# Performance work log

Measured on AMD Instinct MI355X. Metric: run time of the kernel, lower is better.

## Reference

```python
import jax, jax.numpy as jnp
import numpy as np

B, T = 4, 32768
NM = 80      # n_mels
RC = 120     # residual_channels
SC = 240     # skip_channels
NB = 16      # num_blocks
ND = 8       # num_dilations
NC = 256     # num_classes


def setup_inputs() -> dict:
    key = jax.random.key(0)
    ks = jax.random.split(key, 18)
    s = 0.05
    return {
        "wav": jax.random.normal(ks[0], (B, 1, T), dtype=jnp.float32),
        "cond": jax.random.normal(ks[1], (B, NM, T), dtype=jnp.float32),
        "wav_w": jax.random.normal(ks[2], (RC, 1)) * s,
        "wav_b": jnp.zeros((RC,), jnp.float32),
        "cond_w": jax.random.normal(ks[3], (NB, 2 * RC, NM)) * s,
        "cond_b": jnp.zeros((NB, 2 * RC), jnp.float32),
        "dil_w": jax.random.normal(ks[4], (NB, 2 * RC, RC, 2)) * s,
        "dil_b": jnp.zeros((NB, 2 * RC), jnp.float32),
        "skip_w": jax.random.normal(ks[5], (NB, SC, RC)) * s,
        "skip_b": jnp.zeros((NB, SC), jnp.float32),
        "res_w": jax.random.normal(ks[6], (NB, RC, RC)) * s,
        "res_b": jnp.zeros((NB, RC), jnp.float32),
        "out_w": jax.random.normal(ks[7], (NC, SC)) * s,
        "out_b": jnp.zeros((NC,), jnp.float32),
        "end_w": jax.random.normal(ks[8], (NC, NC)) * s,
        "end_b": jnp.zeros((NC,), jnp.float32),
    }


def _conv1x1(w, b, x):
    # w: [O, I], x: [B, I, T] -> [B, O, T]
    return jnp.einsum('oi,bit->bot', w, x) + b[:, None]


def reference(wav, cond, wav_w, wav_b, cond_w, cond_b, dil_w, dil_b,
              skip_w, skip_b, res_w, res_b, out_w, out_b, end_w, end_b):
    Tlen = wav.shape[-1]
    res = _conv1x1(wav_w, wav_b, wav)                      # [B, RC, T]
    skip_sum = jnp.zeros((wav.shape[0], SC, Tlen), wav.dtype)
    for i in range(NB):
        d = 2 ** (i % ND)
        # torch: Conv1d(k=2, dilation=d, padding=d) then [:, :, :-d] == causal conv
        # out[t] = W0 @ x[t-d] + W1 @ x[t]
        x_shift = jnp.pad(res, ((0, 0), (0, 0), (d, 0)))[:, :, :Tlen]
        g = (jnp.einsum('oi,bit->bot', dil_w[i, :, :, 0], x_shift)
             + jnp.einsum('oi,bit->bot', dil_w[i, :, :, 1], res)
             + dil_b[i][:, None]
             + _conv1x1(cond_w[i], cond_b[i], cond))        # [B, 2*RC, T]
        # first RC channels -> tanh branch, second RC -> sigmoid branch
        out = jnp.tanh(g[:, :RC]) * jax.nn.sigmoid(g[:, RC:])
        skip_sum = skip_sum + _conv1x1(skip_w[i], skip_b[i], out)
        res = _conv1x1(res_w[i], res_b[i], out) + res
    o = _conv1x1(out_w, out_b, jax.nn.relu(skip_sum))       # [B, NC, T]
    end = _conv1x1(end_w, end_b, jax.nn.relu(o))            # [B, NC, T]
    return end
```

## Files before the change

kernel.cpp:

```cpp
#include <hip/hip_runtime.h>
#include <hip/hip_fp16.h>


#define BSZ  4
#define TLEN 32768
#define NMEL 80
#define RCH  120
#define SCH  240
#define NBLK 16
#define NCLS 256
#define CP   128
#define CC   96
#define TSB  128
#define TSF  64
#define OUTS 136
#define XES  264

typedef __attribute__((ext_vector_type(8))) short short8;
typedef __attribute__((ext_vector_type(4))) float floatx4;
#define MFMA16 __builtin_amdgcn_mfma_f32_16x16x32_bf16

__device__ __forceinline__ float bf2f(unsigned short u) {
    return __uint_as_float(((unsigned)u) << 16);
}
__device__ __forceinline__ unsigned short f2bf(float f) {
    unsigned x = __float_as_uint(f);
    return (unsigned short)((x + 0x7fffu + ((x >> 16) & 1u)) >> 16);
}
__device__ __forceinline__ float h2f(unsigned short u) {
    return __half2float(__ushort_as_half(u));
}
__device__ __forceinline__ unsigned short f2h(float f) {
    return __half_as_ushort(__float2half(f));
}
__device__ __forceinline__ float tanh_ap(float x) {
    x = fminf(fmaxf(x, -18.f), 18.f);
    float e = __expf(2.f * x);
    return (e - 1.f) / (e + 1.f);
}
__device__ __forceinline__ float sigm_ap(float x) {
    x = fminf(fmaxf(x, -30.f), 30.f);
    return 1.f / (1.f + __expf(-x));
}

#define FR_BLK   257
#define FR_TOT   4368
#define NWELEM   (FR_TOT * 512)
#define BIA_BLK  608
#define NBELEM   (NBLK * BIA_BLK + 512)

__global__ void k_packw(const float* __restrict__ dil_w, const float* __restrict__ cond_w,
                        const float* __restrict__ skip_w, const float* __restrict__ res_w,
                        const float* __restrict__ out_w,  const float* __restrict__ end_w,
                        unsigned short* __restrict__ dst) {
    int idx = blockIdx.x * 256 + threadIdx.x;
    if (idx >= NWELEM) return;
    int fid = idx >> 9;
    int r   = idx & 511;
    int lane = r >> 3, j = r & 7;
    int m16 = lane & 15, q = lane >> 4;
    float v = 0.f;
    if (fid < NBLK * FR_BLK) {
        int blk = fid / FR_BLK, f = fid % FR_BLK;
        if (f < 165) {
            int mt = f / 11, ks = f % 11;
            int row = 16 * mt + m16;
            int kk  = ks * 32 + q * 8 + j;
            int c = row >> 1, br = row & 1;
            int srow = c + 120 * br;
            if (kk < 128) {
                if (kk < 120) v = dil_w[((size_t)(blk * 240 + srow) * 120 + kk) * 2 + 0];
            } else if (kk < 256) {
                int ch = kk - 128;
                if (ch < 120) v = dil_w[((size_t)(blk * 240 + srow) * 120 + ch) * 2 + 1];
            } else {
                int ch = kk - 256;
                if (ch < 80) v = cond_w[(size_t)(blk * 240 + srow) * 80 + ch];
            }
        } else if (f < 225) {
            int f2 = f - 165, mt = f2 / 4, ks = f2 % 4;
            int row = 16 * mt + m16;
            int kk = ks * 32 + q * 8 + j;
            if (kk < 120) v = skip_w[(size_t)(blk * 240 + row) * 120 + kk];
        } else {
            int f2 = f - 225, mt = f2 / 4, ks = f2 % 4;
            int row = 16 * mt + m16;
            int kk = ks * 32 + q * 8 + j;
            if (row < 120 && kk < 120) v = res_w[(size_t)(blk * 120 + row) * 120 + kk];
        }
    } else if (fid < NBLK * FR_BLK + 128) {
        int f = fid - NBLK * FR_BLK, mt = f / 8, ks = f % 8;
        int row = 16 * mt + m16;
        int kk = ks * 32 + q * 8 + j;
        if (kk < 240) v = out_w[(size_t)row * 240 + kk];
    } else {
        int f = fid - NBLK * FR_BLK - 128, mt = f / 8, ks = f % 8;
        int row = 16 * mt + m16;
        int kk = ks * 32 + q * 8 + j;
        v = end_w[(size_t)row * 256 + kk];
    }
    dst[idx] = f2bf(v);
}

__global__ void k_packb(const float* __restrict__ dil_b, const float* __restrict__ cond_b,
                        const float* __restrict__ skip_b, const float* __restrict__ res_b,
                        const float* __restrict__ out_b,  const float* __restrict__ end_b,
                        float* __restrict__ dst) {
    int idx = blockIdx.x * 256 + threadIdx.x;
    if (idx >= NBELEM) return;
    float v;
    if (idx < NBLK * BIA_BLK) {
        int blk = idx / BIA_BLK, f = idx % BIA_BLK;
        if (f < 240) {
            int c = f >> 1, br = f & 1;
            int srow = c + 120 * br;
            v = dil_b[blk * 240 + srow] + cond_b[blk * 240 + srow];
        } else if (f < 480) {
            v = skip_b[blk * 240 + (f - 240)];
        } else {
            int rr = f - 480;
            v = rr < 120 ? res_b[blk * 120 + rr] : 0.f;
        }
    } else {
        int f = idx - NBLK * BIA_BLK;
        v = f < 256 ? out_b[f] : end_b[f - 256];
    }
    dst[idx] = v;
}

__global__ void k_init2(const float* __restrict__ wav, const float* __restrict__ wav_w,
                        const float* __restrict__ wav_b, unsigned short* __restrict__ res) {
    int idx = blockIdx.x * 256 + threadIdx.x;
    float wv = wav[idx];
    unsigned* dst = (unsigned*)(res + (size_t)idx * CP);
#pragma unroll
    for (int c = 0; c < RCH; c += 2) {
        float v0 = wav_w[c] * wv + wav_b[c];
        float v1 = wav_w[c + 1] * wv + wav_b[c + 1];
        dst[c >> 1] = (unsigned)f2bf(v0) | ((unsigned)f2bf(v1) << 16);
    }
#pragma unroll
    for (int c = RCH; c < CP; c += 2) dst[c >> 1] = 0u;
}

__global__ __launch_bounds__(256) void k_packc(const float* __restrict__ cond,
                                               unsigned short* __restrict__ dst) {
    __shared__ unsigned short CT[64 * CC];
    const int tid = threadIdx.x;
    const int t0 = blockIdx.x * 64;
    const int b = blockIdx.y;
    for (int i = tid; i < NMEL * 64; i += 256) {
        int c = i >> 6, tt = i & 63;
        CT[tt * CC + c] = f2bf(cond[((size_t)b * NMEL + c) * TLEN + t0 + tt]);
    }
    for (int i = tid; i < (CC - NMEL) * 64; i += 256) {
        int c = NMEL + (i >> 6), tt = i & 63;
        CT[tt * CC + c] = 0;
    }
    __syncthreads();
    unsigned* dp = (unsigned*)(dst + ((size_t)b * TLEN + t0) * CC);
    const unsigned* sp = (const unsigned*)CT;
    for (int i = tid; i < 64 * (CC / 2); i += 256) dp[i] = sp[i];
}

template <bool HF>
__global__ __launch_bounds__(256, 2) void k_block4(
    const unsigned short* __restrict__ resIn,
    unsigned short* __restrict__ resOut,
    const unsigned short* __restrict__ condp,
    void* __restrict__ skipPtr,
    const unsigned short* __restrict__ wp,
    const float* __restrict__ bp,
    int d) {
    __shared__ __align__(16) unsigned short OUT[TSB * OUTS];
    __shared__ __align__(16) float BIAS[BIA_BLK];

    const int tid = threadIdx.x;
    const int lane = tid & 63;
    const int n = lane & 15, q = lane >> 4;
    const int w = __builtin_amdgcn_readfirstlane(tid >> 6);
    const int t0 = blockIdx.x * TSB;
    const int b = blockIdx.y;
    const size_t bT = (size_t)b * TLEN;

    for (int i = tid; i < BIA_BLK; i += 256) BIAS[i] = bp[i];
    for (int i = tid; i < TSB * 8; i += 256) {
        int col = i >> 3, ch = RCH + (i & 7);
        OUT[col * OUTS + ch] = 0;
    }

    const int mtb = w * 4;
    const int mtn = (w == 3) ? 3 : 4;
    const unsigned short* resb = resIn + bT * CP;
    const unsigned short* conb = condp + bT * CC;

    floatx4 acc[4][8];
#pragma unroll
    for (int mi = 0; mi < 4; mi++)
#pragma unroll
        for (int nt = 0; nt < 8; nt++) acc[mi][nt] = (floatx4){0.f, 0.f, 0.f, 0.f};

    for (int ks = 0; ks < 11; ks++) {
        short8 Bf[8];
        if (ks < 8) {
            const int dd = (ks < 4) ? d : 0;
            const int kl = (ks & 3) * 32 + q * 8;
            if (t0 >= TSB || dd == 0) {
#pragma unroll
                for (int nt = 0; nt < 8; nt++) {
                    int t = t0 + nt * 16 + n - dd;
                    Bf[nt] = *(const short8*)(resb + (size_t)t * CP + kl);
                }
            } else {
#pragma unroll
                for (int nt = 0; nt < 8; nt++) {
                    int t = t0 + nt * 16 + n - dd;
                    int tc = t < 0 ? 0 : t;
                    short8 v = *(const short8*)(resb + (size_t)tc * CP + kl);
                    if (t < 0) v = (short8){0, 0, 0, 0, 0, 0, 0, 0};
                    Bf[nt] = v;
                }
            }
        } else {
            const int kl = (ks - 8) * 32 + q * 8;
#pragma unroll
            for (int nt = 0; nt < 8; nt++) {
                int t = t0 + nt * 16 + n;
                Bf[nt] = *(const short8*)(conb + (size_t)t * CC + kl);
            }
        }
#pragma unroll
        for (int mi = 0; mi < 4; mi++) {
            if (mi < mtn) {
                short8 A = *(const short8*)(wp + ((size_t)((mtb + mi) * 11 + ks) * 64 + lane) * 8);
#pragma unroll
                for (int nt = 0; nt < 8; nt++)
                    acc[mi][nt] = MFMA16(A, Bf[nt], acc[mi][nt], 0, 0, 0);
            }
        }
    }

#pragma unroll
    for (int mi = 0; mi < 4; mi++) {
        if (mi < mtn) {
            int mt = mtb + mi;
            int p0 = 16 * mt + 4 * q;
            int ch = 8 * mt + 2 * q;
            float bt0 = BIAS[p0], bs0 = BIAS[p0 + 1];
            float bt1 = BIAS[p0 + 2], bs1 = BIAS[p0 + 3];
#pragma unroll
            for (int nt = 0; nt < 8; nt++) {
                int col = nt * 16 + n;
                float o0 = tanh_ap(acc[mi][nt][0] + bt0) * sigm_ap(acc[mi][nt][1] + bs0);
                float o1 = tanh_ap(acc[mi][nt][2] + bt1) * sigm_ap(acc[mi][nt][3] + bs1);
                *(unsigned*)&OUT[col * OUTS + ch] =
                    (unsigned)f2bf(o0) | ((unsigned)f2bf(o1) << 16);
            }
        }
    }
    __syncthreads();

    {
        floatx4 acS[4][8];
#pragma unroll
        for (int mi = 0; mi < 4; mi++)
#pragma unroll
            for (int nt = 0; nt < 8; nt++) acS[mi][nt] = (floatx4){0.f, 0.f, 0.f, 0.f};
        for (int ks = 0; ks < 4; ks++) {
            short8 Bf[8];
#pragma unroll
            for (int nt = 0; nt < 8; nt++) {
                int col = nt * 16 + n;
                Bf[nt] = *(const short8*)&OUT[col * OUTS + ks * 32 + q * 8];
            }
#pragma unroll
            for (int mi = 0; mi < 4; mi++) {
                if (mi < mtn) {
                    short8 A = *(const short8*)(wp + ((size_t)(165 + (mtb + mi) * 4 + ks) * 64 + lane) * 8);
#pragma unroll
                    for (int nt = 0; nt < 8; nt++)
                        acS[mi][nt] = MFMA16(A, Bf[nt], acS[mi][nt], 0, 0, 0);
                }
            }
        }
#pragma unroll
        for (int mi = 0; mi < 4; mi++) {
            if (mi < mtn) {
                int mt = mtb + mi;
                int r0 = 16 * mt + 4 * q;
                floatx4 bb = *(const floatx4*)&BIAS[240 + r0];
#pragma unroll
                for (int nt = 0; nt < 8; nt++) {
                    int t = t0 + nt * 16 + n;
                    if (HF) {
                        unsigned short* sp = (unsigned short*)skipPtr +
                            ((size_t)(b * SCH) + r0) * TLEN + t;
#pragma unroll
                        for (int r = 0; r < 4; r++) {
                            size_t off = (size_t)r * TLEN;
                            sp[off] = f2h(h2f(sp[off]) + acS[mi][nt][r] + bb[r]);
                        }
                    } else {
                        float* sp = (float*)skipPtr + ((size_t)(b * NCLS) + r0) * TLEN + t;
#pragma unroll
                        for (int r = 0; r < 4; r++)
                            sp[(size_t)r * TLEN] += acS[mi][nt][r] + bb[r];
                    }
                }
            }
        }
    }

    {
        floatx4 acR[2][8];
#pragma unroll
        for (int mi = 0; mi < 2; mi++)
#pragma unroll
            for (int nt = 0; nt < 8; nt++) acR[mi][nt] = (floatx4){0.f, 0.f, 0.f, 0.f};
        for (int ks = 0; ks < 4; ks++) {
            short8 Bf[8];
#pragma unroll
            for (int nt = 0; nt < 8; nt++) {
                int col = nt * 16 + n;
                Bf[nt] = *(const short8*)&OUT[col * OUTS + ks * 32 + q * 8];
            }
#pragma unroll
            for (int mi = 0; mi < 2; mi++) {
                short8 A = *(const short8*)(wp + ((size_t)(225 + (2 * w + mi) * 4 + ks) * 64 + lane) * 8);
#pragma unroll
                for (int nt = 0; nt < 8; nt++)
                    acR[mi][nt] = MFMA16(A, Bf[nt], acR[mi][nt], 0, 0, 0);
            }
        }
#pragma unroll
        for (int mi = 0; mi < 2; mi++) {
            int mt = 2 * w + mi;
            int r0 = 16 * mt + 4 * q;
            bool pad = (r0 >= RCH);
            floatx4 bb = *(const floatx4*)&BIAS[480 + r0];
#pragma unroll
            for (int nt = 0; nt < 8; nt++) {
                int t = t0 + nt * 16 + n;
                const unsigned short* rip = resIn + (bT + t) * CP + r0;
                unsigned short* rop = resOut + (bT + t) * CP + r0;
                uint2 ri = *(const uint2*)rip;
                float v0 = acR[mi][nt][0] + bb[0] + bf2f((unsigned short)(ri.x & 0xffff));
                float v1 = acR[mi][nt][1] + bb[1] + bf2f((unsigned short)(ri.x >> 16));
                float v2 = acR[mi][nt][2] + bb[2] + bf2f((unsigned short)(ri.y & 0xffff));
                float v3 = acR[mi][nt][3] + bb[3] + bf2f((unsigned short)(ri.y >> 16));
                uint2 ov;
                ov.x = pad ? 0u : ((unsigned)f2bf(v0) | ((unsigned)f2bf(v1) << 16));
                ov.y = pad ? 0u : ((unsigned)f2bf(v2) | ((unsigned)f2bf(v3) << 16));
                *(uint2*)rop = ov;
            }
        }
    }
}

template <bool HF>
__global__ __launch_bounds__(256, 2) void k_final4(
    const void* __restrict__ skipPtr,
    float* __restrict__ io,
    const unsigned short* __restrict__ wpO,
    const unsigned short* __restrict__ wpE,
    const float* __restrict__ bpF) {
    __shared__ __align__(16) unsigned short X[TSF * XES];
    __shared__ __align__(16) unsigned short E[TSF * XES];
    __shared__ float BF[512];

    const int tid = threadIdx.x;
    const int lane = tid & 63;
    const int n = lane & 15, q = lane >> 4;
    const int w = __builtin_amdgcn_readfirstlane(tid >> 6);
    const int t0 = blockIdx.x * TSF;
    const int b = blockIdx.y;

    for (int i = tid; i < 512; i += 256) BF[i] = bpF[i];
    for (int i = tid; i < SCH * TSF; i += 256) {
        int row = i >> 6, col = i & 63;
        float v;
        if (HF) v = h2f(((const unsigned short*)skipPtr)[((size_t)(b * SCH) + row) * TLEN + t0 + col]);
        else    v = io[((size_t)(b * NCLS) + row) * TLEN + t0 + col];
        X[col * XES + row] = f2bf(fmaxf(v, 0.f));
    }
    for (int i = tid; i < (NCLS - SCH) * TSF; i += 256) {
        int row = SCH + (i >> 6), col = i & 63;
        X[col * XES + row] = 0;
    }
    __syncthreads();

    const int mtb = w * 4;
    {
        floatx4 acc[4][4];
#pragma unroll
        for (int mi = 0; mi < 4; mi++)
#pragma unroll
            for (int nt = 0; nt < 4; nt++) acc[mi][nt] = (floatx4){0.f, 0.f, 0.f, 0.f};
        for (int ks = 0; ks < 8; ks++) {
            short8 Bf[4];
#pragma unroll
            for (int nt = 0; nt < 4; nt++) {
                int col = nt * 16 + n;
                Bf[nt] = *(const short8*)&X[col * XES + ks * 32 + q * 8];
            }
#pragma unroll
            for (int mi = 0; mi < 4; mi++) {
                short8 A = *(const short8*)(wpO + ((size_t)((mtb + mi) * 8 + ks) * 64 + lane) * 8);
#pragma unroll
                for (int nt = 0; nt < 4; nt++)
                    acc[mi][nt] = MFMA16(A, Bf[nt], acc[mi][nt], 0, 0, 0);
            }
        }
#pragma unroll
        for (int mi = 0; mi < 4; mi++) {
            int ch0 = 16 * (mtb + mi) + 4 * q;
#pragma unroll
            for (int nt = 0; nt < 4; nt++) {
                int col = nt * 16 + n;
                float v0 = fmaxf(acc[mi][nt][0] + BF[ch0], 0.f);
                float v1 = fmaxf(acc[mi][nt][1] + BF[ch0 + 1], 0.f);
                float v2 = fmaxf(acc[mi][nt][2] + BF[ch0 + 2], 0.f);
                float v3 = fmaxf(acc[mi][nt][3] + BF[ch0 + 3], 0.f);
                *(unsigned*)&E[col * XES + ch0] = (unsigned)f2bf(v0) | ((unsigned)f2bf(v1) << 16);
                *(unsigned*)&E[col * XES + ch0 + 2] = (unsigned)f2bf(v2) | ((unsigned)f2bf(v3) << 16);
            }
        }
    }
    __syncthreads();
    {
        floatx4 acc[4][4];
#pragma unroll
        for (int mi = 0; mi < 4; mi++)
#pragma unroll
            for (int nt = 0; nt < 4; nt++) acc[mi][nt] = (floatx4){0.f, 0.f, 0.f, 0.f};
        for (int ks = 0; ks < 8; ks++) {
            short8 Bf[4];
#pragma unroll
            for (int nt = 0; nt < 4; nt++) {
                int col = nt * 16 + n;
                Bf[nt] = *(const short8*)&E[col * XES + ks * 32 + q * 8];
            }
#pragma unroll
            for (int mi = 0; mi < 4; mi++) {
                short8 A = *(const short8*)(wpE + ((size_t)((mtb + mi) * 8 + ks) * 64 + lane) * 8);
#pragma unroll
                for (int nt = 0; nt < 4; nt++)
                    acc[mi][nt] = MFMA16(A, Bf[nt], acc[mi][nt], 0, 0, 0);
            }
        }
#pragma unroll
        for (int mi = 0; mi < 4; mi++) {
            int r0 = 16 * (mtb + mi) + 4 * q;
#pragma unroll
            for (int nt = 0; nt < 4; nt++) {
                int t = t0 + nt * 16 + n;
#pragma unroll
                for (int r = 0; r < 4; r++)
                    io[((size_t)(b * NCLS) + r0 + r) * TLEN + t] =
                        acc[mi][nt][r] + BF[256 + r0 + r];
            }
        }
    }
}

extern "C" void kernel_launch(void* const* d_in, const int* in_sizes, int n_in,
                              void* d_out, int out_size, void* d_ws, size_t ws_size,
                              hipStream_t stream) {
    (void)in_sizes; (void)n_in;
    const float* wav    = (const float*)d_in[0];
    const float* cond   = (const float*)d_in[1];
    const float* wav_w  = (const float*)d_in[2];
    const float* wav_b  = (const float*)d_in[3];
    const float* cond_w = (const float*)d_in[4];
    const float* cond_b = (const float*)d_in[5];
    const float* dil_w  = (const float*)d_in[6];
    const float* dil_b  = (const float*)d_in[7];
    const float* skip_w = (const float*)d_in[8];
    const float* skip_b = (const float*)d_in[9];
    const float* res_w  = (const float*)d_in[10];
    const float* res_b  = (const float*)d_in[11];
    const float* out_w  = (const float*)d_in[12];
    const float* out_b  = (const float*)d_in[13];
    const float* end_w  = (const float*)d_in[14];
    const float* end_b  = (const float*)d_in[15];

    const size_t resElems = (size_t)BSZ * TLEN * CP;
    unsigned short* resA  = (unsigned short*)d_ws;
    unsigned short* resB  = resA + resElems;
    unsigned short* condp = resB + resElems;
    unsigned short* wp    = condp + (size_t)BSZ * TLEN * CC;
    float* bp             = (float*)(wp + (size_t)FR_TOT * 512);
    unsigned short* skipH = (unsigned short*)(bp + NBELEM);
    const size_t skipHBytes = (size_t)BSZ * SCH * TLEN * 2;
    const size_t needA = (size_t)((char*)(skipH) - (char*)d_ws) + skipHBytes;
    const bool hf = ws_size >= needA;

    void* skipPtr = hf ? (void*)skipH : (void*)d_out;
    if (hf) hipMemsetAsync(skipH, 0, skipHBytes, stream);
    else    hipMemsetAsync(d_out, 0, (size_t)out_size * sizeof(float), stream);

    k_packw<<<dim3((NWELEM + 255) / 256), 256, 0, stream>>>(
        dil_w, cond_w, skip_w, res_w, out_w, end_w, wp);
    k_packb<<<dim3((NBELEM + 255) / 256), 256, 0, stream>>>(
        dil_b, cond_b, skip_b, res_b, out_b, end_b, bp);
    k_init2<<<dim3(BSZ * TLEN / 256), 256, 0, stream>>>(wav, wav_w, wav_b, resA);
    k_packc<<<dim3(TLEN / 64, BSZ), 256, 0, stream>>>(cond, condp);

    unsigned short* rin = resA;
    unsigned short* rout = resB;
    for (int i = 0; i < NBLK; i++) {
        int d = 1 << (i & 7);
        if (hf)
            k_block4<true><<<dim3(TLEN / TSB, BSZ), 256, 0, stream>>>(
                rin, rout, condp, skipPtr,
                wp + (size_t)i * FR_BLK * 512, bp + (size_t)i * BIA_BLK, d);
        else
            k_block4<false><<<dim3(TLEN / TSB, BSZ), 256, 0, stream>>>(
                rin, rout, condp, skipPtr,
                wp + (size_t)i * FR_BLK * 512, bp + (size_t)i * BIA_BLK, d);
        unsigned short* tmp = rin; rin = rout; rout = tmp;
    }
    if (hf)
        k_final4<true><<<dim3(TLEN / TSF, BSZ), 256, 0, stream>>>(
            skipPtr, (float*)d_out,
            wp + (size_t)(NBLK * FR_BLK) * 512,
            wp + (size_t)(NBLK * FR_BLK + 128) * 512,
            bp + NBLK * BIA_BLK);
    else
        k_final4<false><<<dim3(TLEN / TSF, BSZ), 256, 0, stream>>>(
            skipPtr, (float*)d_out,
            wp + (size_t)(NBLK * FR_BLK) * 512,
            wp + (size_t)(NBLK * FR_BLK + 128) * 512,
            bp + NBLK * BIA_BLK);
}
```

Baseline: 1.861 ms.

## Split block kernel into half-tiles, swizzle tile order, store fp16 skip time-major

The residual-block kernel now processes its 128-step tile as two 64-step halves, shrinking accumulator arrays so launch bounds can request four waves per SIMD instead of two. Block indices are remapped so neighbouring blocks work on distant tiles. The fp16 skip accumulator changes from channel-major to time-major, so each lane does one 8-byte read-modify-write instead of four strided 2-byte accesses, and the final kernel reads that layout vectorised. The risks are extra barriers and register pressure under the higher occupancy target, and the host code and any skip initialisation must match the new layout.

```diff
diff --git a/kernel.cpp b/kernel.cpp
--- a/kernel.cpp
+++ b/kernel.cpp
@@ -164,7 +164,7 @@
 }
 
 template <bool HF>
-__global__ __launch_bounds__(256, 2) void k_block4(
+__global__ __launch_bounds__(256, 4) void k_block4(
     const unsigned short* __restrict__ resIn,
     unsigned short* __restrict__ resOut,
     const unsigned short* __restrict__ condp,
@@ -179,7 +179,9 @@
     const int lane = tid & 63;
     const int n = lane & 15, q = lane >> 4;
     const int w = __builtin_amdgcn_readfirstlane(tid >> 6);
-    const int t0 = blockIdx.x * TSB;
+    const int bx = blockIdx.x;
+    const int tile = ((bx & 7) << 5) | (bx >> 3);
+    const int t0 = tile * TSB;
     const int b = blockIdx.y;
     const size_t bT = (size_t)b * TLEN;
 
@@ -194,164 +196,173 @@
     const unsigned short* resb = resIn + bT * CP;
     const unsigned short* conb = condp + bT * CC;
 
-    floatx4 acc[4][8];
-#pragma unroll
-    for (int mi = 0; mi < 4; mi++)
-#pragma unroll
-        for (int nt = 0; nt < 8; nt++) acc[mi][nt] = (floatx4){0.f, 0.f, 0.f, 0.f};
-
-    for (int ks = 0; ks < 11; ks++) {
-        short8 Bf[8];
-        if (ks < 8) {
-            const int dd = (ks < 4) ? d : 0;
-            const int kl = (ks & 3) * 32 + q * 8;
-            if (t0 >= TSB || dd == 0) {
-#pragma unroll
-                for (int nt = 0; nt < 8; nt++) {
-                    int t = t0 + nt * 16 + n - dd;
-                    Bf[nt] = *(const short8*)(resb + (size_t)t * CP + kl);
+#pragma unroll 1
+    for (int h = 0; h < 2; ++h) {
+        const int tb = t0 + h * 64;
+
+        floatx4 acc[4][4];
+#pragma unroll
+        for (int mi = 0; mi < 4; mi++)
+#pragma unroll
+            for (int nt = 0; nt < 4; nt++) acc[mi][nt] = (floatx4){0.f, 0.f, 0.f, 0.f};
+
+        for (int ks = 0; ks < 11; ks++) {
+            short8 Bf[4];
+            if (ks < 8) {
+                const int dd = (ks < 4) ? d : 0;
+                const int kl = (ks & 3) * 32 + q * 8;
+                if (t0 >= TSB || dd == 0) {
+#pragma unroll
+                    for (int nt = 0; nt < 4; nt++) {
+                        int t = tb + nt * 16 + n - dd;
+                        Bf[nt] = *(const short8*)(resb + (size_t)t * CP + kl);
+                    }
+                } else {
+#pragma unroll
+                    for (int nt = 0; nt < 4; nt++) {
+                        int t = tb + nt * 16 + n - dd;
+                        int tc = t < 0 ? 0 : t;
+                        short8 v = *(const short8*)(resb + (size_t)tc * CP + kl);
+                        if (t < 0) v = (short8){0, 0, 0, 0, 0, 0, 0, 0};
+                        Bf[nt] = v;
+                    }
                 }
             } else {
-#pragma unroll
-                for (int nt = 0; nt < 8; nt++) {
-                    int t = t0 + nt * 16 + n - dd;
-                    int tc = t < 0 ? 0 : t;
-                    short8 v = *(const short8*)(resb + (size_t)tc * CP + kl);
-                    if (t < 0) v = (short8){0, 0, 0, 0, 0, 0, 0, 0};
-                    Bf[nt] = v;
-                }
-            }
-        } else {
-            const int kl = (ks - 8) * 32 + q * 8;
-#pragma unroll
-            for (int nt = 0; nt < 8; nt++) {
-                int t = t0 + nt * 16 + n;
-                Bf[nt] = *(const short8*)(conb + (size_t)t * CC + kl);
-            }
-        }
-#pragma unroll
-        for (int mi = 0; mi < 4; mi++) {
-            if (mi < mtn) {
-                short8 A = *(const short8*)(wp + ((size_t)((mtb + mi) * 11 + ks) * 64 + lane) * 8);
-#pragma unroll
-                for (int nt = 0; nt < 8; nt++)
-                    acc[mi][nt] = MFMA16(A, Bf[nt], acc[mi][nt], 0, 0, 0);
-            }
-        }
-    }
-
-#pragma unroll
-    for (int mi = 0; mi < 4; mi++) {
-        if (mi < mtn) {
-            int mt = mtb + mi;
-            int p0 = 16 * mt + 4 * q;
-            int ch = 8 * mt + 2 * q;
-            float bt0 = BIAS[p0], bs0 = BIAS[p0 + 1];
-            float bt1 = BIAS[p0 + 2], bs1 = BIAS[p0 + 3];
-#pragma unroll
-            for (int nt = 0; nt < 8; nt++) {
-                int col = nt * 16 + n;
-                float o0 = tanh_ap(acc[mi][nt][0] + bt0) * sigm_ap(acc[mi][nt][1] + bs0);
-                float o1 = tanh_ap(acc[mi][nt][2] + bt1) * sigm_ap(acc[mi][nt][3] + bs1);
-                *(unsigned*)&OUT[col * OUTS + ch] =
-                    (unsigned)f2bf(o0) | ((unsigned)f2bf(o1) << 16);
-            }
-        }
-    }
-    __syncthreads();
-
-    {
-        floatx4 acS[4][8];
-#pragma unroll
-        for (int mi = 0; mi < 4; mi++)
-#pragma unroll
-            for (int nt = 0; nt < 8; nt++) acS[mi][nt] = (floatx4){0.f, 0.f, 0.f, 0.f};
-        for (int ks = 0; ks < 4; ks++) {
-            short8 Bf[8];
-#pragma unroll
-            for (int nt = 0; nt < 8; nt++) {
-                int col = nt * 16 + n;
-                Bf[nt] = *(const short8*)&OUT[col * OUTS + ks * 32 + q * 8];
+                const int kl = (ks - 8) * 32 + q * 8;
+#pragma unroll
+                for (int nt = 0; nt < 4; nt++) {
+                    int t = tb + nt * 16 + n;
+                    Bf[nt] = *(const short8*)(conb + (size_t)t * CC + kl);
+                }
             }
 #pragma unroll
             for (int mi = 0; mi < 4; mi++) {
                 if (mi < mtn) {
-                    short8 A = *(const short8*)(wp + ((size_t)(165 + (mtb + mi) * 4 + ks) * 64 + lane) * 8);
-#pragma unroll
-                    for (int nt = 0; nt < 8; nt++)
-                        acS[mi][nt] = MFMA16(A, Bf[nt], acS[mi][nt], 0, 0, 0);
-                }
-            }
-        }
+                    short8 A = *(const short8*)(wp + ((size_t)((mtb + mi) * 11 + ks) * 64 + lane) * 8);
+#pragma unroll
+                    for (int nt = 0; nt < 4; nt++)
+                        acc[mi][nt] = MFMA16(A, Bf[nt], acc[mi][nt], 0, 0, 0);
+                }
+            }
+        }
+
 #pragma unroll
         for (int mi = 0; mi < 4; mi++) {
             if (mi < mtn) {
                 int mt = mtb + mi;
+                int p0 = 16 * mt + 4 * q;
+                int ch = 8 * mt + 2 * q;
+                float bt0 = BIAS[p0], bs0 = BIAS[p0 + 1];
+                float bt1 = BIAS[p0 + 2], bs1 = BIAS[p0 + 3];
+#pragma unroll
+                for (int nt = 0; nt < 4; nt++) {
+                    int col = h * 64 + nt * 16 + n;
+                    float o0 = tanh_ap(acc[mi][nt][0] + bt0) * sigm_ap(acc[mi][nt][1] + bs0);
+                    float o1 = tanh_ap(acc[mi][nt][2] + bt1) * sigm_ap(acc[mi][nt][3] + bs1);
+                    *(unsigned*)&OUT[col * OUTS + ch] =
+                        (unsigned)f2bf(o0) | ((unsigned)f2bf(o1) << 16);
+                }
+            }
+        }
+        __syncthreads();
+
+        {
+            floatx4 acS[4][4];
+#pragma unroll
+            for (int mi = 0; mi < 4; mi++)
+#pragma unroll
+                for (int nt = 0; nt < 4; nt++) acS[mi][nt] = (floatx4){0.f, 0.f, 0.f, 0.f};
+            for (int ks = 0; ks < 4; ks++) {
+                short8 Bf[4];
+#pragma unroll
+                for (int nt = 0; nt < 4; nt++) {
+                    int col = h * 64 + nt * 16 + n;
+                    Bf[nt] = *(const short8*)&OUT[col * OUTS + ks * 32 + q * 8];
+                }
+#pragma unroll
+                for (int mi = 0; mi < 4; mi++) {
+                    if (mi < mtn) {
+                        short8 A = *(const short8*)(wp + ((size_t)(165 + (mtb + mi) * 4 + ks) * 64 + lane) * 8);
+#pragma unroll
+                        for (int nt = 0; nt < 4; nt++)
+                            acS[mi][nt] = MFMA16(A, Bf[nt], acS[mi][nt], 0, 0, 0);
+                    }
+                }
+            }
+#pragma unroll
+            for (int mi = 0; mi < 4; mi++) {
+                if (mi < mtn) {
+                    int mt = mtb + mi;
+                    int r0 = 16 * mt + 4 * q;
+                    floatx4 bb = *(const floatx4*)&BIAS[240 + r0];
+#pragma unroll
+                    for (int nt = 0; nt < 4; nt++) {
+                        int t = tb + nt * 16 + n;
+                        if (HF) {
+                            unsigned short* sp = (unsigned short*)skipPtr +
+                                (bT + (size_t)t) * SCH + r0;
+                            uint2 sv = *(const uint2*)sp;
+                            float v0 = h2f((unsigned short)(sv.x & 0xffff)) + acS[mi][nt][0] + bb[0];
+                            float v1 = h2f((unsigned short)(sv.x >> 16))    + acS[mi][nt][1] + bb[1];
+                            float v2 = h2f((unsigned short)(sv.y & 0xffff)) + acS[mi][nt][2] + bb[2];
+                            float v3 = h2f((unsigned short)(sv.y >> 16))    + acS[mi][nt][3] + bb[3];
+                            uint2 ov;
+                            ov.x = (unsigned)f2h(v0) | ((unsigned)f2h(v1) << 16);
+                            ov.y = (unsigned)f2h(v2) | ((unsigned)f2h(v3) << 16);
+                            *(uint2*)sp = ov;
+                        } else {
+                            float* sp = (float*)skipPtr + ((size_t)(b * NCLS) + r0) * TLEN + t;
+#pragma unroll
+                            for (int r = 0; r < 4; r++)
+                                sp[(size_t)r * TLEN] += acS[mi][nt][r] + bb[r];
+                        }
+                    }
+                }
+            }
+        }
+
+        {
+            floatx4 acR[2][4];
+#pragma unroll
+            for (int mi = 0; mi < 2; mi++)
+#pragma unroll
+                for (int nt = 0; nt < 4; nt++) acR[mi][nt] = (floatx4){0.f, 0.f, 0.f, 0.f};
+            for (int ks = 0; ks < 4; ks++) {
+                short8 Bf[4];
+#pragma unroll
+                for (int nt = 0; nt < 4; nt++) {
+                    int col = h * 64 + nt * 16 + n;
+                    Bf[nt] = *(const short8*)&OUT[col * OUTS + ks * 32 + q * 8];
+                }
+#pragma unroll
+                for (int mi = 0; mi < 2; mi++) {
+                    short8 A = *(const short8*)(wp + ((size_t)(225 + (2 * w + mi) * 4 + ks) * 64 + lane) * 8);
+#pragma unroll
+                    for (int nt = 0; nt < 4; nt++)
+                        acR[mi][nt] = MFMA16(A, Bf[nt], acR[mi][nt], 0, 0, 0);
+                }
+            }
+#pragma unroll
+            for (int mi = 0; mi < 2; mi++) {
+                int mt = 2 * w + mi;
                 int r0 = 16 * mt + 4 * q;
-                floatx4 bb = *(const floatx4*)&BIAS[240 + r0];
-#pragma unroll
-                for (int nt = 0; nt < 8; nt++) {
-                    int t = t0 + nt * 16 + n;
-                    if (HF) {
-                        unsigned short* sp = (unsigned short*)skipPtr +
-                            ((size_t)(b * SCH) + r0) * TLEN + t;
-#pragma unroll
-                        for (int r = 0; r < 4; r++) {
-                            size_t off = (size_t)r * TLEN;
-                            sp[off] = f2h(h2f(sp[off]) + acS[mi][nt][r] + bb[r]);
-                        }
-                    } else {
-                        float* sp = (float*)skipPtr + ((size_t)(b * NCLS) + r0) * TLEN + t;
-#pragma unroll
-                        for (int r = 0; r < 4; r++)
-                            sp[(size_t)r * TLEN] += acS[mi][nt][r] + bb[r];
-                    }
-                }
-            }
-        }
-    }
-
-    {
-        floatx4 acR[2][8];
-#pragma unroll
-        for (int mi = 0; mi < 2; mi++)
-#pragma unroll
-            for (int nt = 0; nt < 8; nt++) acR[mi][nt] = (floatx4){0.f, 0.f, 0.f, 0.f};
-        for (int ks = 0; ks < 4; ks++) {
-            short8 Bf[8];
-#pragma unroll
-            for (int nt = 0; nt < 8; nt++) {
-                int col = nt * 16 + n;
-                Bf[nt] = *(const short8*)&OUT[col * OUTS + ks * 32 + q * 8];
-            }
-#pragma unroll
-            for (int mi = 0; mi < 2; mi++) {
-                short8 A = *(const short8*)(wp + ((size_t)(225 + (2 * w + mi) * 4 + ks) * 64 + lane) * 8);
-#pragma unroll
-                for (int nt = 0; nt < 8; nt++)
-                    acR[mi][nt] = MFMA16(A, Bf[nt], acR[mi][nt], 0, 0, 0);
-            }
-        }
-#pragma unroll
-        for (int mi = 0; mi < 2; mi++) {
-            int mt = 2 * w + mi;
-            int r0 = 16 * mt + 4 * q;
-            bool pad = (r0 >= RCH);
-            floatx4 bb = *(const floatx4*)&BIAS[480 + r0];
-#pragma unroll
-            for (int nt = 0; nt < 8; nt++) {
-                int t = t0 + nt * 16 + n;
-                const unsigned short* rip = resIn + (bT + t) * CP + r0;
-                unsigned short* rop = resOut + (bT + t) * CP + r0;
-                uint2 ri = *(const uint2*)rip;
-                float v0 = acR[mi][nt][0] + bb[0] + bf2f((unsigned short)(ri.x & 0xffff));
-                float v1 = acR[mi][nt][1] + bb[1] + bf2f((unsigned short)(ri.x >> 16));
-                float v2 = acR[mi][nt][2] + bb[2] + bf2f((unsigned short)(ri.y & 0xffff));
-                float v3 = acR[mi][nt][3] + bb[3] + bf2f((unsigned short)(ri.y >> 16));
-                uint2 ov;
-                ov.x = pad ? 0u : ((unsigned)f2bf(v0) | ((unsigned)f2bf(v1) << 16));
-                ov.y = pad ? 0u : ((unsigned)f2bf(v2) | ((unsigned)f2bf(v3) << 16));
-                *(uint2*)rop = ov;
+                bool pad = (r0 >= RCH);
+                floatx4 bb = *(const floatx4*)&BIAS[480 + r0];
+#pragma unroll
+                for (int nt = 0; nt < 4; nt++) {
+                    int t = tb + nt * 16 + n;
+                    const unsigned short* rip = resIn + (bT + t) * CP + r0;
+                    unsigned short* rop = resOut + (bT + t) * CP + r0;
+                    uint2 ri = *(const uint2*)rip;
+                    float v0 = acR[mi][nt][0] + bb[0] + bf2f((unsigned short)(ri.x & 0xffff));
+                    float v1 = acR[mi][nt][1] + bb[1] + bf2f((unsigned short)(ri.x >> 16));
+                    float v2 = acR[mi][nt][2] + bb[2] + bf2f((unsigned short)(ri.y & 0xffff));
+                    float v3 = acR[mi][nt][3] + bb[3] + bf2f((unsigned short)(ri.y >> 16));
+                    uint2 ov;
+                    ov.x = pad ? 0u : ((unsigned)f2bf(v0) | ((unsigned)f2bf(v1) << 16));
+                    ov.y = pad ? 0u : ((unsigned)f2bf(v2) | ((unsigned)f2bf(v3) << 16));
+                    *(uint2*)rop = ov;
+                }
             }
         }
     }
@@ -376,12 +387,25 @@
     const int b = blockIdx.y;
 
     for (int i = tid; i < 512; i += 256) BF[i] = bpF[i];
-    for (int i = tid; i < SCH * TSF; i += 256) {
-        int row = i >> 6, col = i & 63;
-        float v;
-        if (HF) v = h2f(((const unsigned short*)skipPtr)[((size_t)(b * SCH) + row) * TLEN + t0 + col]);
-        else    v = io[((size_t)(b * NCLS) + row) * TLEN + t0 + col];
-        X[col * XES + row] = f2bf(fmaxf(v, 0.f));
+    if (HF) {
+        for (int i = tid; i < TSF * (SCH / 4); i += 256) {
+            int col = i / 60, c4 = (i - col * 60) * 4;
+            const unsigned short* sp = (const unsigned short*)skipPtr +
+                ((size_t)(b * TLEN) + t0 + col) * SCH + c4;
+            uint2 v = *(const uint2*)sp;
+            float f0 = fmaxf(h2f((unsigned short)(v.x & 0xffff)), 0.f);
+            float f1 = fmaxf(h2f((unsigned short)(v.x >> 16)), 0.f);
+            float f2 = fmaxf(h2f((unsigned short)(v.y & 0xffff)), 0.f);
+            float f3 = fmaxf(h2f((unsigned short)(v.y >> 16)), 0.f);
+            *(unsigned*)&X[col * XES + c4]     = (unsigned)f2bf(f0) | ((unsigned)f2bf(f1) << 16);
+            *(unsigned*)&X[col * XES + c4 + 2] = (unsigned)f2bf(f2) | ((unsigned)f2bf(f3) << 16);
+        }
+    } else {
+        for (int i = tid; i < SCH * TSF; i += 256) {
+            int row = i >> 6, col = i & 63;
+            float vv = io[((size_t)(b * NCLS) + row) * TLEN + t0 + col];
+            X[col * XES + row] = f2bf(fmaxf(vv, 0.f));
+        }
     }
     for (int i = tid; i < (NCLS - SCH) * TSF; i += 256) {
         int row = SCH + (i >> 6), col = i & 63;
```

New measurement: 5.498 ms. 195% more time.

## Split block GEMM into two M-halves and skip the skip-buffer memset

Applied to the files above, without the earlier changes.

The gated and skip GEMMs now run in two passes, each over 2 M-tiles per wave instead of 4, roughly halving the accumulator registers. The min-blocks-per-CU hint is dropped from launch bounds. The first residual block writes the fp16 skip buffer directly instead of reading and adding, so the memset of that buffer is removed. The two-pass split reloads the B fragments from global memory twice, trading extra loads for lower register pressure.

```diff
diff --git a/kernel.cpp b/kernel.cpp
--- a/kernel.cpp
+++ b/kernel.cpp
@@ -163,8 +163,8 @@
     for (int i = tid; i < 64 * (CC / 2); i += 256) dp[i] = sp[i];
 }
 
-template <bool HF>
-__global__ __launch_bounds__(256, 2) void k_block4(
+template <bool HF, bool FIRST>
+__global__ __launch_bounds__(256) void k_block4(
     const unsigned short* __restrict__ resIn,
     unsigned short* __restrict__ resOut,
     const unsigned short* __restrict__ condp,
@@ -189,81 +189,86 @@
         OUT[col * OUTS + ch] = 0;
     }
 
-    const int mtb = w * 4;
-    const int mtn = (w == 3) ? 3 : 4;
     const unsigned short* resb = resIn + bT * CP;
     const unsigned short* conb = condp + bT * CC;
 
-    floatx4 acc[4][8];
-#pragma unroll
-    for (int mi = 0; mi < 4; mi++)
-#pragma unroll
-        for (int nt = 0; nt < 8; nt++) acc[mi][nt] = (floatx4){0.f, 0.f, 0.f, 0.f};
-
-    for (int ks = 0; ks < 11; ks++) {
-        short8 Bf[8];
-        if (ks < 8) {
-            const int dd = (ks < 4) ? d : 0;
-            const int kl = (ks & 3) * 32 + q * 8;
-            if (t0 >= TSB || dd == 0) {
-#pragma unroll
-                for (int nt = 0; nt < 8; nt++) {
-                    int t = t0 + nt * 16 + n - dd;
-                    Bf[nt] = *(const short8*)(resb + (size_t)t * CP + kl);
+#pragma unroll 1
+    for (int mh = 0; mh < 2; ++mh) {
+        const int mtb = mh * 8 + w * 2;
+        floatx4 acc[2][8];
+#pragma unroll
+        for (int mi = 0; mi < 2; mi++)
+#pragma unroll
+            for (int nt = 0; nt < 8; nt++) acc[mi][nt] = (floatx4){0.f, 0.f, 0.f, 0.f};
+
+        for (int ks = 0; ks < 11; ks++) {
+            short8 Bf[8];
+            if (ks < 8) {
+                const int dd = (ks < 4) ? d : 0;
+                const int kl = (ks & 3) * 32 + q * 8;
+                if (t0 >= TSB || dd == 0) {
+#pragma unroll
+                    for (int nt = 0; nt < 8; nt++) {
+                        int t = t0 + nt * 16 + n - dd;
+                        Bf[nt] = *(const short8*)(resb + (size_t)t * CP + kl);
+                    }
+                } else {
+#pragma unroll
+                    for (int nt = 0; nt < 8; nt++) {
+                        int t = t0 + nt * 16 + n - dd;
+                        int tc = t < 0 ? 0 : t;
+                        short8 v = *(const short8*)(resb + (size_t)tc * CP + kl);
+                        if (t < 0) v = (short8){0, 0, 0, 0, 0, 0, 0, 0};
+                        Bf[nt] = v;
+                    }
                 }
             } else {
+                const int kl = (ks - 8) * 32 + q * 8;
 #pragma unroll
                 for (int nt = 0; nt < 8; nt++) {
-                    int t = t0 + nt * 16 + n - dd;
-                    int tc = t < 0 ? 0 : t;
-                    short8 v = *(const short8*)(resb + (size_t)tc * CP + kl);
-                    if (t < 0) v = (short8){0, 0, 0, 0, 0, 0, 0, 0};
-                    Bf[nt] = v;
+                    int t = t0 + nt * 16 + n;
+                    Bf[nt] = *(const short8*)(conb + (size_t)t * CC + kl);
                 }
             }
-        } else {
-            const int kl = (ks - 8) * 32 + q * 8;
-#pragma unroll
-            for (int nt = 0; nt < 8; nt++) {
-                int t = t0 + nt * 16 + n;
-                Bf[nt] = *(const short8*)(conb + (size_t)t * CC + kl);
-            }
-        }
-#pragma unroll
-        for (int mi = 0; mi < 4; mi++) {
-            if (mi < mtn) {
-                short8 A = *(const short8*)(wp + ((size_t)((mtb + mi) * 11 + ks) * 64 + lane) * 8);
-#pragma unroll
-                for (int nt = 0; nt < 8; nt++)
-                    acc[mi][nt] = MFMA16(A, Bf[nt], acc[mi][nt], 0, 0, 0);
-            }
-        }
-    }
-
-#pragma unroll
-    for (int mi = 0; mi < 4; mi++) {
-        if (mi < mtn) {
+#pragma unroll
+            for (int mi = 0; mi < 2; mi++) {
+                int mt = mtb + mi;
+                if (mt < 15) {
+                    short8 A = *(const short8*)(wp + ((size_t)(mt * 11 + ks) * 64 + lane) * 8);
+#pragma unroll
+                    for (int nt = 0; nt < 8; nt++)
+                        acc[mi][nt] = MFMA16(A, Bf[nt], acc[mi][nt], 0, 0, 0);
+                }
+            }
+        }
+
+#pragma unroll
+        for (int mi = 0; mi < 2; mi++) {
             int mt = mtb + mi;
-            int p0 = 16 * mt + 4 * q;
-            int ch = 8 * mt + 2 * q;
-            float bt0 = BIAS[p0], bs0 = BIAS[p0 + 1];
-            float bt1 = BIAS[p0 + 2], bs1 = BIAS[p0 + 3];
-#pragma unroll
-            for (int nt = 0; nt < 8; nt++) {
-                int col = nt * 16 + n;
-                float o0 = tanh_ap(acc[mi][nt][0] + bt0) * sigm_ap(acc[mi][nt][1] + bs0);
-                float o1 = tanh_ap(acc[mi][nt][2] + bt1) * sigm_ap(acc[mi][nt][3] + bs1);
-                *(unsigned*)&OUT[col * OUTS + ch] =
-                    (unsigned)f2bf(o0) | ((unsigned)f2bf(o1) << 16);
+            if (mt < 15) {
+                int p0 = 16 * mt + 4 * q;
+                int ch = 8 * mt + 2 * q;
+                float bt0 = BIAS[p0], bs0 = BIAS[p0 + 1];
+                float bt1 = BIAS[p0 + 2], bs1 = BIAS[p0 + 3];
+#pragma unroll
+                for (int nt = 0; nt < 8; nt++) {
+                    int col = nt * 16 + n;
+                    float o0 = tanh_ap(acc[mi][nt][0] + bt0) * sigm_ap(acc[mi][nt][1] + bs0);
+                    float o1 = tanh_ap(acc[mi][nt][2] + bt1) * sigm_ap(acc[mi][nt][3] + bs1);
+                    *(unsigned*)&OUT[col * OUTS + ch] =
+                        (unsigned)f2bf(o0) | ((unsigned)f2bf(o1) << 16);
+                }
             }
         }
     }
     __syncthreads();
 
-    {
-        floatx4 acS[4][8];
-#pragma unroll
-        for (int mi = 0; mi < 4; mi++)
+#pragma unroll 1
+    for (int mh = 0; mh < 2; ++mh) {
+        const int mtb = mh * 8 + w * 2;
+        floatx4 acS[2][8];
+#pragma unroll
+        for (int mi = 0; mi < 2; mi++)
 #pragma unroll
             for (int nt = 0; nt < 8; nt++) acS[mi][nt] = (floatx4){0.f, 0.f, 0.f, 0.f};
         for (int ks = 0; ks < 4; ks++) {
@@ -274,9 +279,10 @@
                 Bf[nt] = *(const short8*)&OUT[col * OUTS + ks * 32 + q * 8];
             }
 #pragma unroll
-            for (int mi = 0; mi < 4; mi++) {
-                if (mi < mtn) {
-                    short8 A = *(const short8*)(wp + ((size_t)(165 + (mtb + mi) * 4 + ks) * 64 + lane) * 8);
+            for (int mi = 0; mi < 2; mi++) {
+                int mt = mtb + mi;
+                if (mt < 15) {
+                    short8 A = *(const short8*)(wp + ((size_t)(165 + mt * 4 + ks) * 64 + lane) * 8);
 #pragma unroll
                     for (int nt = 0; nt < 8; nt++)
                         acS[mi][nt] = MFMA16(A, Bf[nt], acS[mi][nt], 0, 0, 0);
@@ -284,9 +290,9 @@
             }
         }
 #pragma unroll
-        for (int mi = 0; mi < 4; mi++) {
-            if (mi < mtn) {
-                int mt = mtb + mi;
+        for (int mi = 0; mi < 2; mi++) {
+            int mt = mtb + mi;
+            if (mt < 15) {
                 int r0 = 16 * mt + 4 * q;
                 floatx4 bb = *(const floatx4*)&BIAS[240 + r0];
 #pragma unroll
@@ -298,7 +304,9 @@
 #pragma unroll
                         for (int r = 0; r < 4; r++) {
                             size_t off = (size_t)r * TLEN;
-                            sp[off] = f2h(h2f(sp[off]) + acS[mi][nt][r] + bb[r]);
+                            float v = acS[mi][nt][r] + bb[r];
+                            if (!FIRST) v += h2f(sp[off]);
+                            sp[off] = f2h(v);
                         }
                     } else {
                         float* sp = (float*)skipPtr + ((size_t)(b * NCLS) + r0) * TLEN + t;
@@ -496,8 +504,7 @@
     const bool hf = ws_size >= needA;
 
     void* skipPtr = hf ? (void*)skipH : (void*)d_out;
-    if (hf) hipMemsetAsync(skipH, 0, skipHBytes, stream);
-    else    hipMemsetAsync(d_out, 0, (size_t)out_size * sizeof(float), stream);
+    if (!hf) hipMemsetAsync(d_out, 0, (size_t)out_size * sizeof(float), stream);
 
     k_packw<<<dim3((NWELEM + 255) / 256), 256, 0, stream>>>(
         dil_w, cond_w, skip_w, res_w, out_w, end_w, wp);
@@ -510,14 +517,20 @@
     unsigned short* rout = resB;
     for (int i = 0; i < NBLK; i++) {
         int d = 1 << (i & 7);
-        if (hf)
-            k_block4<true><<<dim3(TLEN / TSB, BSZ), 256, 0, stream>>>(
+        if (hf) {
+            if (i == 0)
+                k_block4<true, true><<<dim3(TLEN / TSB, BSZ), 256, 0, stream>>>(
+                    rin, rout, condp, skipPtr,
+                    wp + (size_t)i * FR_BLK * 512, bp + (size_t)i * BIA_BLK, d);
+            else
+                k_block4<true, false><<<dim3(TLEN / TSB, BSZ), 256, 0, stream>>>(
+                    rin, rout, condp, skipPtr,
+                    wp + (size_t)i * FR_BLK * 512, bp + (size_t)i * BIA_BLK, d);
+        } else {
+            k_block4<false, false><<<dim3(TLEN / TSB, BSZ), 256, 0, stream>>>(
                 rin, rout, condp, skipPtr,
                 wp + (size_t)i * FR_BLK * 512, bp + (size_t)i * BIA_BLK, d);
-        else
-            k_block4<false><<<dim3(TLEN / TSB, BSZ), 256, 0, stream>>>(
-                rin, rout, condp, skipPtr,
-                wp + (size_t)i * FR_BLK * 512, bp + (size_t)i * BIA_BLK, d);
+        }
         unsigned short* tmp = rin; rin = rout; rout = tmp;
     }
     if (hf)
```

Result: slower. 3.307 ms (+77.7%).

## Store fp16 skip accumulator time-major with vectorized 8-byte accesses, skip memset

Applied to the files above, without the earlier changes.

Switches the fp16 skip-sum buffer from channel-major [B,SCH,T] to time-major [B,T,SCH], so each lane's four consecutive channel rows become one 8-byte load and store instead of four strided 2-byte accesses. The first block writes the skip value without reading it, which removes the need for a memset of the skip buffer. The final kernel reads the new layout with vectorized loads and writes packed pairs into shared memory. In exchange, a wavefront's stores are now spread across rows of stride SCH in time, which may reduce coalescing across lanes.

```diff
diff --git a/kernel.cpp b/kernel.cpp
--- a/kernel.cpp
+++ b/kernel.cpp
@@ -163,7 +163,7 @@
     for (int i = tid; i < 64 * (CC / 2); i += 256) dp[i] = sp[i];
 }
 
-template <bool HF>
+template <bool HF, bool FIRST>
 __global__ __launch_bounds__(256, 2) void k_block4(
     const unsigned short* __restrict__ resIn,
     unsigned short* __restrict__ resOut,
@@ -294,12 +294,22 @@
                     int t = t0 + nt * 16 + n;
                     if (HF) {
                         unsigned short* sp = (unsigned short*)skipPtr +
-                            ((size_t)(b * SCH) + r0) * TLEN + t;
-#pragma unroll
-                        for (int r = 0; r < 4; r++) {
-                            size_t off = (size_t)r * TLEN;
-                            sp[off] = f2h(h2f(sp[off]) + acS[mi][nt][r] + bb[r]);
+                            (bT + (size_t)t) * SCH + r0;
+                        float v0 = acS[mi][nt][0] + bb[0];
+                        float v1 = acS[mi][nt][1] + bb[1];
+                        float v2 = acS[mi][nt][2] + bb[2];
+                        float v3 = acS[mi][nt][3] + bb[3];
+                        if (!FIRST) {
+                            uint2 sv = *(const uint2*)sp;
+                            v0 += h2f((unsigned short)(sv.x & 0xffff));
+                            v1 += h2f((unsigned short)(sv.x >> 16));
+                            v2 += h2f((unsigned short)(sv.y & 0xffff));
+                            v3 += h2f((unsigned short)(sv.y >> 16));
                         }
+                        uint2 ov;
+                        ov.x = (unsigned)f2h(v0) | ((unsigned)f2h(v1) << 16);
+                        ov.y = (unsigned)f2h(v2) | ((unsigned)f2h(v3) << 16);
+                        *(uint2*)sp = ov;
                     } else {
                         float* sp = (float*)skipPtr + ((size_t)(b * NCLS) + r0) * TLEN + t;
 #pragma unroll
@@ -376,12 +386,25 @@
     const int b = blockIdx.y;
 
     for (int i = tid; i < 512; i += 256) BF[i] = bpF[i];
-    for (int i = tid; i < SCH * TSF; i += 256) {
-        int row = i >> 6, col = i & 63;
-        float v;
-        if (HF) v = h2f(((const unsigned short*)skipPtr)[((size_t)(b * SCH) + row) * TLEN + t0 + col]);
-        else    v = io[((size_t)(b * NCLS) + row) * TLEN + t0 + col];
-        X[col * XES + row] = f2bf(fmaxf(v, 0.f));
+    if (HF) {
+        for (int i = tid; i < TSF * (SCH / 4); i += 256) {
+            int col = i / (SCH / 4), c4 = (i - col * (SCH / 4)) * 4;
+            const unsigned short* sp = (const unsigned short*)skipPtr +
+                ((size_t)(b * TLEN) + t0 + col) * SCH + c4;
+            uint2 v = *(const uint2*)sp;
+            float f0 = fmaxf(h2f((unsigned short)(v.x & 0xffff)), 0.f);
+            float f1 = fmaxf(h2f((unsigned short)(v.x >> 16)), 0.f);
+            float f2 = fmaxf(h2f((unsigned short)(v.y & 0xffff)), 0.f);
+            float f3 = fmaxf(h2f((unsigned short)(v.y >> 16)), 0.f);
+            *(unsigned*)&X[col * XES + c4]     = (unsigned)f2bf(f0) | ((unsigned)f2bf(f1) << 16);
+            *(unsigned*)&X[col * XES + c4 + 2] = (unsigned)f2bf(f2) | ((unsigned)f2bf(f3) << 16);
+        }
+    } else {
+        for (int i = tid; i < SCH * TSF; i += 256) {
+            int row = i >> 6, col = i & 63;
+            float v = io[((size_t)(b * NCLS) + row) * TLEN + t0 + col];
+            X[col * XES + row] = f2bf(fmaxf(v, 0.f));
+        }
     }
     for (int i = tid; i < (NCLS - SCH) * TSF; i += 256) {
         int row = SCH + (i >> 6), col = i & 63;
@@ -496,8 +519,7 @@
     const bool hf = ws_size >= needA;
 
     void* skipPtr = hf ? (void*)skipH : (void*)d_out;
-    if (hf) hipMemsetAsync(skipH, 0, skipHBytes, stream);
-    else    hipMemsetAsync(d_out, 0, (size_t)out_size * sizeof(float), stream);
+    if (!hf) hipMemsetAsync(d_out, 0, (size_t)out_size * sizeof(float), stream);
 
     k_packw<<<dim3((NWELEM + 255) / 256), 256, 0, stream>>>(
         dil_w, cond_w, skip_w, res_w, out_w, end_w, wp);
@@ -510,14 +532,20 @@
     unsigned short* rout = resB;
     for (int i = 0; i < NBLK; i++) {
         int d = 1 << (i & 7);
-        if (hf)
-            k_block4<true><<<dim3(TLEN / TSB, BSZ), 256, 0, stream>>>(
+        if (hf) {
+            if (i == 0)
+                k_block4<true, true><<<dim3(TLEN / TSB, BSZ), 256, 0, stream>>>(
+                    rin, rout, condp, skipPtr,
+                    wp + (size_t)i * FR_BLK * 512, bp + (size_t)i * BIA_BLK, d);
+            else
+                k_block4<true, false><<<dim3(TLEN / TSB, BSZ), 256, 0, stream>>>(
+                    rin, rout, condp, skipPtr,
+                    wp + (size_t)i * FR_BLK * 512, bp + (size_t)i * BIA_BLK, d);
+        } else {
+            k_block4<false, false><<<dim3(TLEN / TSB, BSZ), 256, 0, stream>>>(
                 rin, rout, condp, skipPtr,
                 wp + (size_t)i * FR_BLK * 512, bp + (size_t)i * BIA_BLK, d);
-        else
-            k_block4<false><<<dim3(TLEN / TSB, BSZ), 256, 0, stream>>>(
-                rin, rout, condp, skipPtr,
-                wp + (size_t)i * FR_BLK * 512, bp + (size_t)i * BIA_BLK, d);
+        }
         unsigned short* tmp = rin; rin = rout; rout = tmp;
     }
     if (hf)
```

After: 2.060 ms. 1.11x slower.
